# Kernel tuning notes

Measured on AMD Instinct MI355X. Metric: run time of the kernel, lower is better.

Reference implementation:

```python
import jax, jax.numpy as jnp
import numpy as np

D_MODEL, D_K, D_V, H = 1024, 128, 128, 8


def setup_inputs() -> dict:
    key = jax.random.key(0)
    ks = jax.random.split(key, 14)
    B, NQ, NK = 8, 1024, 1024
    def lin(kw, out_d, in_d):
        # xavier_uniform weight, zero bias
        lim = jnp.sqrt(6.0 / (in_d + out_d))
        return jax.random.uniform(kw, (out_d, in_d), jnp.float32, -lim, lim)
    return {
        "queries": jax.random.normal(ks[0], (B, NQ, D_MODEL), jnp.float32),
        "keys": jax.random.normal(ks[1], (B, NK, D_MODEL), jnp.float32),
        "values": jax.random.normal(ks[2], (B, NK, D_MODEL), jnp.float32),
        "language_signals": jax.random.normal(ks[3], (B, NQ, D_MODEL), jnp.float32),
        "Wq": lin(ks[4], H * D_K, D_MODEL), "bq": jnp.zeros((H * D_K,), jnp.float32),
        "Wk": lin(ks[5], H * D_K, D_MODEL), "bk": jnp.zeros((H * D_K,), jnp.float32),
        "Wv": lin(ks[6], H * D_V, D_MODEL), "bv": jnp.zeros((H * D_V,), jnp.float32),
        "Ws": lin(ks[7], H * D_K, D_MODEL), "bs": jnp.zeros((H * D_K,), jnp.float32),
        "Wo": lin(ks[8], D_MODEL, H * D_V), "bo": jnp.zeros((D_MODEL,), jnp.float32),
    }


def reference(queries, keys, values, language_signals,
              Wq, bq, Wk, bk, Wv, bv, Ws, bs, Wo, bo):
    b, nq, _ = queries.shape
    nk = keys.shape[1]
    scale = 1.0 / jnp.sqrt(jnp.asarray(D_K, queries.dtype))
    # project and split heads -> (b, h, n, d)
    q = (queries @ Wq.T + bq).reshape(b, nq, H, D_K).transpose(0, 2, 1, 3)
    s = (language_signals @ Ws.T + bs).reshape(b, nq, H, D_K).transpose(0, 2, 1, 3)
    k = (keys @ Wk.T + bk).reshape(b, nk, H, D_K).transpose(0, 2, 1, 3)
    v = (values @ Wv.T + bv).reshape(b, nk, H, D_V).transpose(0, 2, 1, 3)
    attn = jnp.einsum('bhqd,bhkd->bhqk', q, k) * scale           # (b,h,nq,nk)
    lang = jnp.einsum('bhqd,bhqd->bhq', q, s) * scale            # diagonal sentinel score
    combined = jnp.concatenate([attn, lang[..., None]], axis=-1)  # (b,h,nq,nk+1)
    p = jax.nn.softmax(combined, axis=-1)
    # per-query value set is [v; s_i]: split matmul into kv part + sentinel part
    out = jnp.einsum('bhqk,bhkd->bhqd', p[..., :nk], v) + p[..., nk:] * s
    out = out.transpose(0, 2, 1, 3).reshape(b, nq, H * D_V)
    return out @ Wo.T + bo
```

## Files before the change

kernel.cpp:

```cpp
#include <hip/hip_runtime.h>
#include <hip/hip_bf16.h>


typedef __attribute__((ext_vector_type(8))) short s16x8;
typedef __attribute__((ext_vector_type(4))) float f32x4;
typedef __attribute__((ext_vector_type(16))) float f32x16;
typedef __attribute__((ext_vector_type(4))) unsigned int u32x4;

#define DEVI static __device__ __forceinline__

constexpr int BATCH = 8;
constexpr int SEQ   = 1024;
constexpr int NH    = 8;
constexpr int DH    = 128;
constexpr int DM    = 1024;

DEVI short bf16r(float f) {
  __hip_bfloat16 h = __float2bfloat16(f);
  return *reinterpret_cast<short*>(&h);
}
DEVI float bf2f(short s) {
  __hip_bfloat16 h;
  *reinterpret_cast<short*>(&h) = s;
  return __bfloat162float(h);
}
DEVI s16x8 cvt8(const float4& a, const float4& b) {
  s16x8 r;
  r[0] = bf16r(a.x); r[1] = bf16r(a.y); r[2] = bf16r(a.z); r[3] = bf16r(a.w);
  r[4] = bf16r(b.x); r[5] = bf16r(b.y); r[6] = bf16r(b.z); r[7] = bf16r(b.w);
  return r;
}
DEVI unsigned int pack2bf(float a, float b) {
  return (unsigned int)(unsigned short)bf16r(a) |
         ((unsigned int)(unsigned short)bf16r(b) << 16);
}

#define GLOAD16(g, l)                                                        \
  __builtin_amdgcn_global_load_lds(                                          \
      (const __attribute__((address_space(1))) unsigned int*)(g),            \
      (__attribute__((address_space(3))) unsigned int*)(l), 16, 0, 0)

DEVI f32x4 mfma(s16x8 a, s16x8 b, f32x4 c) {
  return __builtin_amdgcn_mfma_f32_16x16x32_bf16(a, b, c, 0, 0, 0);
}
DEVI f32x16 mfma32(s16x8 a, s16x8 b, f32x16 c) {
  return __builtin_amdgcn_mfma_f32_32x32x16_bf16(a, b, c, 0, 0, 0);
}

__global__ __launch_bounds__(256)
void cvt_all(const float* __restrict__ a0, const float* __restrict__ a1,
             const float* __restrict__ a2, const float* __restrict__ a3,
             const float* __restrict__ w0, const float* __restrict__ w1,
             const float* __restrict__ w2, const float* __restrict__ w3,
             const float* __restrict__ w4,
             short* __restrict__ d0, short* __restrict__ d1,
             short* __restrict__ d2, short* __restrict__ d3,
             short* __restrict__ e0, short* __restrict__ e1,
             short* __restrict__ e2, short* __restrict__ e3,
             short* __restrict__ e4) {
  const float* s; short* d; int idx;
  int bid = blockIdx.x;
  if (bid < 16384) {
    int which = bid >> 12; idx = bid & 4095;
    switch (which) {
      case 0: s = a0; d = d0; break;
      case 1: s = a1; d = d1; break;
      case 2: s = a2; d = d2; break;
      default: s = a3; d = d3; break;
    }
  } else {
    int r = bid - 16384;
    int which = r >> 9; idx = r & 511;
    switch (which) {
      case 0: s = w0; d = e0; break;
      case 1: s = w1; d = e1; break;
      case 2: s = w2; d = e2; break;
      case 3: s = w3; d = e3; break;
      default: s = w4; d = e4; break;
    }
  }
  size_t i = ((size_t)idx * 256 + threadIdx.x) * 8;
  float4 a = *(const float4*)(s + i);
  float4 b = *(const float4*)(s + i + 4);
  *(s16x8*)(d + i) = cvt8(a, b);
}

DEVI void gemm_core(const short* __restrict__ A, const short* __restrict__ W,
                    short* Alds, short* Blds, int m0, int n0,
                    f32x4 (&acc)[4][4]) {
  const int tid = threadIdx.x, lane = tid & 63, wid = tid >> 6;
  const int wm = wid >> 1, wn = wid & 1, lr = lane & 15, lg = lane >> 4;
  const int srow = wid * 32 + (lane >> 3);
  const int scb  = (lane & 7) * 16;

  for (int k0 = 0; k0 < DM; k0 += 64) {
    if (k0) __syncthreads();
#pragma unroll
    for (int t = 0; t < 4; t++) {
      int row = srow + t * 8;
      int cbs = scb ^ ((row & 7) << 4);
      GLOAD16((const char*)A + ((size_t)(m0 + row) * DM + k0) * 2 + cbs,
              (char*)Alds + wid * 4096 + t * 1024);
      GLOAD16((const char*)W + ((size_t)(n0 + row) * DM + k0) * 2 + cbs,
              (char*)Blds + wid * 4096 + t * 1024);
    }
    __syncthreads();
#pragma unroll
    for (int kk = 0; kk < 2; kk++) {
      s16x8 af[4], bf[4];
#pragma unroll
      for (int i = 0; i < 4; i++) {
        int row = wm * 64 + i * 16 + lr;
        af[i] = *(const s16x8*)((const char*)Alds + row * 128 +
                                ((kk * 64 + lg * 16) ^ ((row & 7) << 4)));
      }
#pragma unroll
      for (int j = 0; j < 4; j++) {
        int row = wn * 64 + j * 16 + lr;
        bf[j] = *(const s16x8*)((const char*)Blds + row * 128 +
                                ((kk * 64 + lg * 16) ^ ((row & 7) << 4)));
      }
#pragma unroll
      for (int i = 0; i < 4; i++)
#pragma unroll
        for (int j = 0; j < 4; j++)
          acc[i][j] = mfma(af[i], bf[j], acc[i][j]);
    }
  }
}

__global__ __launch_bounds__(256)
void proj_gemm(const short* __restrict__ qa, const short* __restrict__ ka,
               const short* __restrict__ va, const short* __restrict__ sa,
               const short* __restrict__ wq, const short* __restrict__ wk,
               const short* __restrict__ wv, const short* __restrict__ wsn,
               const float* __restrict__ bq, const float* __restrict__ bk,
               const float* __restrict__ bv, const float* __restrict__ bsn,
               short* __restrict__ Qo, short* __restrict__ Ko,
               short* __restrict__ Vo, short* __restrict__ So) {
  __shared__ short Alds[128 * 64];
  __shared__ short Blds[128 * 64];
  const int z = blockIdx.z;
  const short* A; const short* W; const float* bias; short* C;
  switch (z) {
    case 0: A = qa; W = wq;  bias = bq;  C = Qo; break;
    case 1: A = ka; W = wk;  bias = bk;  C = Ko; break;
    case 2: A = va; W = wv;  bias = bv;  C = Vo; break;
    default: A = sa; W = wsn; bias = bsn; C = So; break;
  }
  const int m0 = blockIdx.x * 128, n0 = blockIdx.y * 128;
  f32x4 acc[4][4] = {};
  gemm_core(A, W, Alds, Blds, m0, n0, acc);

  const int lane = threadIdx.x & 63, wid = threadIdx.x >> 6;
  const int wm = wid >> 1, wn = wid & 1, lr = lane & 15, lg = lane >> 4;
#pragma unroll
  for (int i = 0; i < 4; i++) {
#pragma unroll
    for (int r = 0; r < 4; r++) {
      int m = m0 + wm * 64 + i * 16 + lg * 4 + r;
      int bb = m >> 10, sq = m & 1023;
#pragma unroll
      for (int j = 0; j < 4; j++) {
        int n = n0 + wn * 64 + j * 16 + lr;
        float v = acc[i][j][r] + bias[n];
        int hh = n >> 7, d = n & 127;
        if (z == 2)
          C[((size_t)(bb * NH + hh) * DH + d) * SEQ + sq] = bf16r(v);
        else
          C[((size_t)(bb * NH + hh) * SEQ + sq) * DH + d] = bf16r(v);
      }
    }
  }
}

__global__ __launch_bounds__(256)
void out_gemm(const short* __restrict__ A, const short* __restrict__ W,
              const float* __restrict__ bias, float* __restrict__ C) {
  __shared__ short Alds[128 * 64];
  __shared__ short Blds[128 * 64];
  const int bid = blockIdx.x;
  const int wg = (bid & 7) * 64 + (bid >> 3);
  const int m0 = (wg >> 3) * 128, n0 = (wg & 7) * 128;
  f32x4 acc[4][4] = {};
  gemm_core(A, W, Alds, Blds, m0, n0, acc);

  const int lane = threadIdx.x & 63, wid = threadIdx.x >> 6;
  const int wm = wid >> 1, wn = wid & 1, lr = lane & 15, lg = lane >> 4;
#pragma unroll
  for (int i = 0; i < 4; i++)
#pragma unroll
    for (int r = 0; r < 4; r++) {
      int m = m0 + wm * 64 + i * 16 + lg * 4 + r;
#pragma unroll
      for (int j = 0; j < 4; j++) {
        int n = n0 + wn * 64 + j * 16 + lr;
        C[(size_t)m * DM + n] = acc[i][j][r] + bias[n];
      }
    }
}

DEVI void stage_kv(const char* Kg, const char* Vg, int k0n,
                   short* Kd, short* Vd, int tid, int wave) {
  const int krow_l = tid >> 4, kslot = tid & 15;
  const int vrow_l = tid >> 3, vslot = tid & 7;
#pragma unroll
  for (int ln = 0; ln < 4; ln++) {
    int kr = ln * 16 + krow_l;
    int ss = kslot ^ (((kr & 7) << 1) ^ ((kr >> 3) & 3));
    GLOAD16(Kg + (size_t)(k0n + kr) * 256 + ss * 16,
            (char*)Kd + ln * 4096 + wave * 1024);
  }
#pragma unroll
  for (int ln = 0; ln < 4; ln++) {
    int dr = ln * 32 + vrow_l;
    int ss = vslot ^ ((dr & 7) ^ ((dr >> 3) & 3));
    GLOAD16(Vg + (size_t)dr * 2048 + (size_t)k0n * 2 + ss * 16,
            (char*)Vd + ln * 4096 + wave * 1024);
  }
}

__global__ __launch_bounds__(256, 2)
void attn_kernel(const short* __restrict__ Qb, const short* __restrict__ Kb,
                 const short* __restrict__ Vtb, const short* __restrict__ Sb,
                 short* __restrict__ att) {
  __shared__ short Klds[2][64 * 128];
  __shared__ short Vtlds[2][128 * 64];

  const int tid = threadIdx.x, lane = tid & 63, wave = tid >> 6;
  const int l31 = lane & 31, hi = lane >> 5;
  const int bid = blockIdx.x;
  const int logical = (bid & 7) * 64 + (bid >> 3);
  const int hb = logical >> 3, qt = logical & 7;
  const int b = hb >> 3, h = hb & 7;
  const int q0 = qt * 128 + wave * 32;
  const size_t base = (size_t)(b * NH + h) * SEQ * DH;
  const char* Kg = (const char*)(Kb + base);
  const char* Vg = (const char*)(Vtb + base);
  const float scale = 0.08838834764831845f * 1.44269504088896340f;

  s16x8 qf[8];
  {
    const char* qrow = (const char*)(Qb + base) + (size_t)(q0 + l31) * 256 + hi * 16;
#pragma unroll
    for (int kd = 0; kd < 8; kd++) qf[kd] = *(const s16x8*)(qrow + kd * 32);
  }

  float m_run = -INFINITY, l_run = 0.f;
  f32x16 oacc[4] = {};

  const int v4r = ((((lane & 7) << 1) ^ ((lane >> 3) & 3))) << 4;
  const int v3r = (((lane & 7) ^ ((lane >> 3) & 3))) << 4;

  stage_kv(Kg, Vg, 0, Klds[0], Vtlds[0], tid, wave);

  for (int it = 0; it < 16; ++it) {
    const int cur = it & 1;
    __syncthreads();
    if (it < 15)
      stage_kv(Kg, Vg, (it + 1) * 64, Klds[cur ^ 1], Vtlds[cur ^ 1], tid, wave);

    f32x16 st0 = {}, st1 = {};
    const char* Kb0 = (const char*)Klds[cur] + l31 * 256;
    __builtin_amdgcn_s_setprio(1);
#pragma unroll
    for (int kd = 0; kd < 8; kd++) {
      int co = (kd * 32 + hi * 16) ^ v4r;
      s16x8 a0 = *(const s16x8*)(Kb0 + co);
      s16x8 a1 = *(const s16x8*)(Kb0 + 32 * 256 + co);
      st0 = mfma32(a0, qf[kd], st0);
      st1 = mfma32(a1, qf[kd], st1);
    }
    __builtin_amdgcn_s_setprio(0);

    float traw = -INFINITY;
#pragma unroll
    for (int r = 0; r < 16; r++) {
      traw = fmaxf(traw, st0[r]);
      traw = fmaxf(traw, st1[r]);
    }
    traw = fmaxf(traw, __shfl_xor(traw, 32));
    float tmax = traw * scale;
    const bool skip = __all(tmax - m_run <= 8.f);
    float m_new = skip ? m_run : fmaxf(m_run, tmax);
    float psum = 0.f;
    unsigned W0[8], W1[8];
#pragma unroll
    for (int i = 0; i < 8; i++) {
      float p0 = exp2f(fmaf(st0[2 * i],     scale, -m_new));
      float p1 = exp2f(fmaf(st0[2 * i + 1], scale, -m_new));
      float p2 = exp2f(fmaf(st1[2 * i],     scale, -m_new));
      float p3 = exp2f(fmaf(st1[2 * i + 1], scale, -m_new));
      psum += (p0 + p1) + (p2 + p3);
      W0[i] = pack2bf(p0, p1);
      W1[i] = pack2bf(p2, p3);
    }
    psum += __shfl_xor(psum, 32);
    if (skip) {
      l_run += psum;
    } else {
      float fac = exp2f(m_run - m_new);
      l_run = l_run * fac + psum;
      m_run = m_new;
#pragma unroll
      for (int reg = 0; reg < 16; reg++) {
        int qs = (reg & 3) + 8 * (reg >> 2);
        float fr = __shfl(fac, qs + 4 * hi);
#pragma unroll
        for (int dt = 0; dt < 4; dt++) oacc[dt][reg] *= fr;
      }
    }

    s16x8 pa[4];
#pragma unroll
    for (int ks = 0; ks < 4; ks++) {
      const int s4 = (ks & 1) * 4;
      unsigned a0, a1, b0, b1;
      if (ks >> 1) { a0 = W1[s4]; a1 = W1[s4 + 1]; b0 = W1[s4 + 2]; b1 = W1[s4 + 3]; }
      else         { a0 = W0[s4]; a1 = W0[s4 + 1]; b0 = W0[s4 + 2]; b1 = W0[s4 + 3]; }
      unsigned snd0 = hi ? a0 : b0, snd1 = hi ? a1 : b1;
      unsigned rem0 = __shfl_xor(snd0, 32), rem1 = __shfl_xor(snd1, 32);
      unsigned w0 = hi ? rem0 : a0;
      unsigned w1 = hi ? rem1 : a1;
      unsigned w2 = hi ? b0 : rem0;
      unsigned w3 = hi ? b1 : rem1;
      u32x4 t4 = {w0, w1, w2, w3};
      pa[ks] = __builtin_bit_cast(s16x8, t4);
    }

    const char* Vb0 = (const char*)Vtlds[cur] + l31 * 128;
    __builtin_amdgcn_s_setprio(1);
#pragma unroll
    for (int dt = 0; dt < 4; dt++) {
#pragma unroll
      for (int ks = 0; ks < 4; ks++) {
        int co = (ks * 32 + hi * 16) ^ v3r;
        s16x8 bv = *(const s16x8*)(Vb0 + dt * 4096 + co);
        oacc[dt] = mfma32(pa[ks], bv, oacc[dt]);
      }
    }
    __builtin_amdgcn_s_setprio(0);
  }

  s16x8 sf[8];
  {
    const char* srow = (const char*)(Sb + base) + (size_t)(q0 + l31) * 256 + hi * 16;
#pragma unroll
    for (int kd = 0; kd < 8; kd++) sf[kd] = *(const s16x8*)(srow + kd * 32);
  }
  float dot = 0.f;
#pragma unroll
  for (int kd = 0; kd < 8; kd++)
#pragma unroll
    for (int j = 0; j < 8; j++) dot += bf2f(qf[kd][j]) * bf2f(sf[kd][j]);
  dot += __shfl_xor(dot, 32);
  float sc = dot * scale;
  float m_new = fmaxf(m_run, sc);
  float fac = exp2f(m_run - m_new);
  float ps = exp2f(sc - m_new);
  l_run = l_run * fac + ps;
  float inv_l = 1.f / l_run;

#pragma unroll
  for (int reg = 0; reg < 16; reg++) {
    int qs = (reg & 3) + 8 * (reg >> 2) + 4 * hi;
    int qsl = (reg & 3) + 8 * (reg >> 2);
    float fr = __shfl(fac,   qsl + 4 * hi);
    float pr = __shfl(ps,    qsl + 4 * hi);
    float il = __shfl(inv_l, qsl + 4 * hi);
    int qg = q0 + qs;
    const short* Sr = Sb + base + (size_t)qg * DH;
    short* orow = att + ((size_t)b * SEQ + qg) * (NH * DH) + h * DH;
#pragma unroll
    for (int dt = 0; dt < 4; dt++) {
      int d = dt * 32 + l31;
      float v = oacc[dt][reg] * fr + pr * bf2f(Sr[d]);
      orow[d] = bf16r(v * il);
    }
  }
}

extern "C" void kernel_launch(void* const* d_in, const int* in_sizes, int n_in,
                              void* d_out, int out_size, void* d_ws, size_t ws_size,
                              hipStream_t stream) {
  const float* queries = (const float*)d_in[0];
  const float* keys    = (const float*)d_in[1];
  const float* values  = (const float*)d_in[2];
  const float* lang    = (const float*)d_in[3];
  const float* Wq = (const float*)d_in[4];  const float* bq = (const float*)d_in[5];
  const float* Wk = (const float*)d_in[6];  const float* bk = (const float*)d_in[7];
  const float* Wv = (const float*)d_in[8];  const float* bv = (const float*)d_in[9];
  const float* Ws = (const float*)d_in[10]; const float* bs = (const float*)d_in[11];
  const float* Wo = (const float*)d_in[12]; const float* bo = (const float*)d_in[13];
  float* out = (float*)d_out;

  short* ws = (short*)d_ws;
  const size_t NE = (size_t)BATCH * SEQ * DM;
  const size_t WE = (size_t)DM * DM;
  short* qbf = ws;
  short* kbf = qbf + NE;
  short* vbf = kbf + NE;
  short* sbf = vbf + NE;
  short* Qb  = sbf + NE;
  short* Kb  = Qb  + NE;
  short* Vtb = Kb  + NE;
  short* Sb  = Vtb + NE;
  short* wqb = Sb  + NE;
  short* wkb = wqb + WE;
  short* wvb = wkb + WE;
  short* wsb = wvb + WE;
  short* wob = wsb + WE;
  short* att = qbf;

  hipLaunchKernelGGL(cvt_all, dim3(16384 + 2560), dim3(256), 0, stream,
                     queries, keys, values, lang, Wq, Wk, Wv, Ws, Wo,
                     qbf, kbf, vbf, sbf, wqb, wkb, wvb, wsb, wob);

  hipLaunchKernelGGL(proj_gemm, dim3(64, 8, 4), dim3(256), 0, stream,
                     qbf, kbf, vbf, sbf, wqb, wkb, wvb, wsb,
                     bq, bk, bv, bs, Qb, Kb, Vtb, Sb);

  hipLaunchKernelGGL(attn_kernel, dim3(512), dim3(256), 0, stream,
                     Qb, Kb, Vtb, Sb, att);

  hipLaunchKernelGGL(out_gemm, dim3(512), dim3(256), 0, stream,
                     att, wob, bo, out);
}
```

Before: 216.8 us.

## Fuse fp32-to-bf16 activation conversion into projection GEMM A-tile loads

Activations are no longer converted to bf16 by a separate pass. The projection GEMM now reads fp32 activation rows directly with vector loads, converts them in registers and writes swizzled bf16 into LDS. The weights are still converted by a smaller kernel. This removes a full write and re-read of four 8x1024x1024 bf16 buffers, but the A loads become synchronous register loads instead of direct-to-LDS loads, and each tile is re-read as fp32 by all 8 N-blocks.

```diff
diff --git a/kernel.cpp b/kernel.cpp
--- a/kernel.cpp
+++ b/kernel.cpp
@@ -48,36 +48,21 @@
 }
 
 __global__ __launch_bounds__(256)
-void cvt_all(const float* __restrict__ a0, const float* __restrict__ a1,
-             const float* __restrict__ a2, const float* __restrict__ a3,
-             const float* __restrict__ w0, const float* __restrict__ w1,
-             const float* __restrict__ w2, const float* __restrict__ w3,
-             const float* __restrict__ w4,
-             short* __restrict__ d0, short* __restrict__ d1,
-             short* __restrict__ d2, short* __restrict__ d3,
-             short* __restrict__ e0, short* __restrict__ e1,
-             short* __restrict__ e2, short* __restrict__ e3,
-             short* __restrict__ e4) {
-  const float* s; short* d; int idx;
+void cvt_w(const float* __restrict__ w0, const float* __restrict__ w1,
+           const float* __restrict__ w2, const float* __restrict__ w3,
+           const float* __restrict__ w4,
+           short* __restrict__ e0, short* __restrict__ e1,
+           short* __restrict__ e2, short* __restrict__ e3,
+           short* __restrict__ e4) {
+  const float* s; short* d;
   int bid = blockIdx.x;
-  if (bid < 16384) {
-    int which = bid >> 12; idx = bid & 4095;
-    switch (which) {
-      case 0: s = a0; d = d0; break;
-      case 1: s = a1; d = d1; break;
-      case 2: s = a2; d = d2; break;
-      default: s = a3; d = d3; break;
-    }
-  } else {
-    int r = bid - 16384;
-    int which = r >> 9; idx = r & 511;
-    switch (which) {
-      case 0: s = w0; d = e0; break;
-      case 1: s = w1; d = e1; break;
-      case 2: s = w2; d = e2; break;
-      case 3: s = w3; d = e3; break;
-      default: s = w4; d = e4; break;
-    }
+  int which = bid >> 9, idx = bid & 511;
+  switch (which) {
+    case 0: s = w0; d = e0; break;
+    case 1: s = w1; d = e1; break;
+    case 2: s = w2; d = e2; break;
+    case 3: s = w3; d = e3; break;
+    default: s = w4; d = e4; break;
   }
   size_t i = ((size_t)idx * 256 + threadIdx.x) * 8;
   float4 a = *(const float4*)(s + i);
@@ -130,8 +115,8 @@
 }
 
 __global__ __launch_bounds__(256)
-void proj_gemm(const short* __restrict__ qa, const short* __restrict__ ka,
-               const short* __restrict__ va, const short* __restrict__ sa,
+void proj_gemm(const float* __restrict__ qa, const float* __restrict__ ka,
+               const float* __restrict__ va, const float* __restrict__ sa,
                const short* __restrict__ wq, const short* __restrict__ wk,
                const short* __restrict__ wv, const short* __restrict__ wsn,
                const float* __restrict__ bq, const float* __restrict__ bk,
@@ -141,7 +126,7 @@
   __shared__ short Alds[128 * 64];
   __shared__ short Blds[128 * 64];
   const int z = blockIdx.z;
-  const short* A; const short* W; const float* bias; short* C;
+  const float* A; const short* W; const float* bias; short* C;
   switch (z) {
     case 0: A = qa; W = wq;  bias = bq;  C = Qo; break;
     case 1: A = ka; W = wk;  bias = bk;  C = Ko; break;
@@ -149,11 +134,65 @@
     default: A = sa; W = wsn; bias = bsn; C = So; break;
   }
   const int m0 = blockIdx.x * 128, n0 = blockIdx.y * 128;
+
+  const int tid = threadIdx.x, lane = tid & 63, wid = tid >> 6;
+  const int wm = wid >> 1, wn = wid & 1, lr = lane & 15, lg = lane >> 4;
+  const int srow = wid * 32 + (lane >> 3);
+  const int scb  = (lane & 7) * 16;
+  const int ar  = tid >> 1;
+  const int ahB = (tid & 1) * 128;
+  const int abh = (tid & 1) * 64;
+  const int asw = (ar & 7) << 4;
+  const char* Arow = (const char*)A + (size_t)(m0 + ar) * 4096;
+  char* Adst = (char*)Alds + ar * 128;
+
   f32x4 acc[4][4] = {};
-  gemm_core(A, W, Alds, Blds, m0, n0, acc);
-
-  const int lane = threadIdx.x & 63, wid = threadIdx.x >> 6;
-  const int wm = wid >> 1, wn = wid & 1, lr = lane & 15, lg = lane >> 4;
+
+  for (int k0 = 0; k0 < DM; k0 += 64) {
+    if (k0) __syncthreads();
+#pragma unroll
+    for (int t = 0; t < 4; t++) {
+      int row = srow + t * 8;
+      int cbs = scb ^ ((row & 7) << 4);
+      GLOAD16((const char*)W + ((size_t)(n0 + row) * DM + k0) * 2 + cbs,
+              (char*)Blds + wid * 4096 + t * 1024);
+    }
+    {
+      float4 av[8];
+      const char* src = Arow + (size_t)k0 * 4 + ahB;
+#pragma unroll
+      for (int j = 0; j < 8; j++)
+        av[j] = *(const float4*)(src + j * 16);
+#pragma unroll
+      for (int c = 0; c < 4; c++) {
+        s16x8 wv8 = cvt8(av[2 * c], av[2 * c + 1]);
+        *(s16x8*)(Adst + ((abh + c * 16) ^ asw)) = wv8;
+      }
+    }
+    __syncthreads();
+#pragma unroll
+    for (int kk = 0; kk < 2; kk++) {
+      s16x8 af[4], bf[4];
+#pragma unroll
+      for (int i = 0; i < 4; i++) {
+        int row = wm * 64 + i * 16 + lr;
+        af[i] = *(const s16x8*)((const char*)Alds + row * 128 +
+                                ((kk * 64 + lg * 16) ^ ((row & 7) << 4)));
+      }
+#pragma unroll
+      for (int j = 0; j < 4; j++) {
+        int row = wn * 64 + j * 16 + lr;
+        bf[j] = *(const s16x8*)((const char*)Blds + row * 128 +
+                                ((kk * 64 + lg * 16) ^ ((row & 7) << 4)));
+      }
+#pragma unroll
+      for (int i = 0; i < 4; i++)
+#pragma unroll
+        for (int j = 0; j < 4; j++)
+          acc[i][j] = mfma(af[i], bf[j], acc[i][j]);
+    }
+  }
+
 #pragma unroll
   for (int i = 0; i < 4; i++) {
 #pragma unroll
@@ -397,11 +436,7 @@
   short* ws = (short*)d_ws;
   const size_t NE = (size_t)BATCH * SEQ * DM;
   const size_t WE = (size_t)DM * DM;
-  short* qbf = ws;
-  short* kbf = qbf + NE;
-  short* vbf = kbf + NE;
-  short* sbf = vbf + NE;
-  short* Qb  = sbf + NE;
+  short* Qb  = ws;
   short* Kb  = Qb  + NE;
   short* Vtb = Kb  + NE;
   short* Sb  = Vtb + NE;
@@ -410,14 +445,13 @@
   short* wvb = wkb + WE;
   short* wsb = wvb + WE;
   short* wob = wsb + WE;
-  short* att = qbf;
-
-  hipLaunchKernelGGL(cvt_all, dim3(16384 + 2560), dim3(256), 0, stream,
-                     queries, keys, values, lang, Wq, Wk, Wv, Ws, Wo,
-                     qbf, kbf, vbf, sbf, wqb, wkb, wvb, wsb, wob);
+  short* att = wob + WE;
+
+  hipLaunchKernelGGL(cvt_w, dim3(2560), dim3(256), 0, stream,
+                     Wq, Wk, Wv, Ws, Wo, wqb, wkb, wvb, wsb, wob);
 
   hipLaunchKernelGGL(proj_gemm, dim3(64, 8, 4), dim3(256), 0, stream,
-                     qbf, kbf, vbf, sbf, wqb, wkb, wvb, wsb,
+                     queries, keys, values, lang, wqb, wkb, wvb, wsb,
                      bq, bk, bv, bs, Qb, Kb, Vtb, Sb);
 
   hipLaunchKernelGGL(attn_kernel, dim3(512), dim3(256), 0, stream,
```

Result: slower. 261.7 us (+20.7%).
